# Performance work log

Measured on AMD Instinct MI355X. Metric: run time of the kernel, lower is better.

The kernel has to match this reference:

```python
import jax, jax.numpy as jnp
import numpy as np

NUM_EMBEDDINGS = 1024
EMBEDDING_DIM = 64
COMMITMENT_COST = 0.25
N_TOKENS = 262144


def setup_inputs() -> dict:
    key = jax.random.key(0)
    k1, k2 = jax.random.split(key)
    inputs = jax.random.normal(k1, (N_TOKENS, EMBEDDING_DIM), dtype=jnp.float32)
    # torch init: uniform(-1/K, 1/K)
    lim = 1.0 / NUM_EMBEDDINGS
    codebook = jax.random.uniform(k2, (NUM_EMBEDDINGS, EMBEDDING_DIM),
                                  dtype=jnp.float32, minval=-lim, maxval=lim)
    return {"inputs": inputs, "codebook": codebook}


def reference(inputs, codebook):
    # inputs: [N, D] flat tokens, codebook: [K, D]
    x = inputs.reshape(-1, EMBEDDING_DIM)
    distances = (jnp.sum(x * x, axis=1, keepdims=True)
                 + jnp.sum(codebook * codebook, axis=1)
                 - 2.0 * jnp.matmul(x, codebook.T))
    encoding_indices = jnp.argmin(distances, axis=1)[:, None]  # [N, 1]
    # one-hot @ codebook == gather of nearest code vectors
    quantized = codebook[encoding_indices[:, 0]]  # [N, D]
    e_latent_loss = jnp.mean((jax.lax.stop_gradient(quantized) - x) ** 2)
    q_latent_loss = jnp.mean((quantized - jax.lax.stop_gradient(x)) ** 2)
    loss = q_latent_loss + COMMITMENT_COST * e_latent_loss
    # straight-through estimator
    quantized = x + jax.lax.stop_gradient(quantized - x)
    return quantized, loss, encoding_indices
```

## Files before the change

kernel.cpp:

```cpp
#include <hip/hip_runtime.h>
#include <math.h>

#define NTOK   262144
#define DIM    64
#define NCODE  1024
#define LOSSOFF (NTOK*DIM)
#define IDXOFF  (NTOK*DIM + 1)

#define MARGIN 4e-5f
#define RCAP   65536

#define OFF_BC     0
#define OFF_CBHI   1024
#define OFF_CBMID  33792
#define OFF_RCNT   66560
#define OFF_CORR   66561
#define OFF_RLIST  66562
#define OFF_BLK    132098
#define WS_FLOATS  134146

typedef __attribute__((ext_vector_type(8))) short short8;
typedef __attribute__((ext_vector_type(4))) float f32x4;

#define GLOAD_LDS(g, l) __builtin_amdgcn_global_load_lds(                    \
    (const __attribute__((address_space(1))) void*)(g),                     \
    (__attribute__((address_space(3))) void*)(l), 16, 0, 0)

__device__ __forceinline__ ushort bf16rn(float f) {
    unsigned u = __float_as_uint(f);
    return (ushort)((u + 0x7fffu + ((u >> 16) & 1u)) >> 16);
}
__device__ __forceinline__ float bf16tof(ushort h) {
    return __uint_as_float(((unsigned)h) << 16);
}

__global__ __launch_bounds__(256) void vq_prep_cb(const float* __restrict__ cb,
                                                  float* __restrict__ ws) {
    int c = blockIdx.x * 256 + threadIdx.x;
    if (c == 0) { ((int*)ws)[OFF_RCNT] = 0; ws[OFF_CORR] = 0.f; }
    if (c >= NCODE) return;
    ushort* cbh = (ushort*)(ws + OFF_CBHI);
    ushort* cbm = (ushort*)(ws + OFF_CBMID);
    const float4* p = (const float4*)(cb + (size_t)c * DIM);
    int sw = (c & 7) << 1;
    float a0 = 0.f, a1 = 0.f, a2 = 0.f, a3 = 0.f;
#pragma unroll
    for (int i = 0; i < 16; i++) {
        float4 v = p[i];
        a0 = fmaf(v.x, v.x, a0); a1 = fmaf(v.y, v.y, a1);
        a2 = fmaf(v.z, v.z, a2); a3 = fmaf(v.w, v.w, a3);
        ushort4 h, m;
        h.x = bf16rn(v.x); m.x = bf16rn(v.x - bf16tof(h.x));
        h.y = bf16rn(v.y); m.y = bf16rn(v.y - bf16tof(h.y));
        h.z = bf16rn(v.z); m.z = bf16rn(v.z - bf16tof(h.z));
        h.w = bf16rn(v.w); m.w = bf16rn(v.w - bf16tof(h.w));
        ((ushort4*)(cbh + (size_t)c * 64))[i ^ sw] = h;
        ((ushort4*)(cbm + (size_t)c * 64))[i ^ sw] = m;
    }
    ws[OFF_BC + c] = (a0 + a1) + (a2 + a3);
}

__global__ __launch_bounds__(256)
__attribute__((amdgpu_waves_per_eu(3)))
void vq_mfma(const float* __restrict__ x,
             const float* __restrict__ cbf,
             float* __restrict__ out,
             float* __restrict__ ws) {
    __shared__ uint4 smem[8][256];
    __shared__ int idxs[128];
    __shared__ float red[4];
    const float* Bc = ws + OFF_BC;
    const ushort* cbh = (const ushort*)(ws + OFF_CBHI);
    const ushort* cbm = (const ushort*)(ws + OFF_CBMID);

    int tid = threadIdx.x, lane = tid & 63, wv = tid >> 6;
    int col = lane & 15, q = lane >> 4, q4 = q * 4;
    int tokb = blockIdx.x * 128 + wv * 32;

    short8 Xhi[2][2], Xmid[2][2];
#pragma unroll
    for (int tt = 0; tt < 2; ++tt) {
        int token = tokb + tt * 16 + col;
        const float* xr = x + (size_t)token * 64;
#pragma unroll
        for (int s = 0; s < 2; ++s) {
            float4 v0 = *(const float4*)(xr + s * 32 + q * 8);
            float4 v1 = *(const float4*)(xr + s * 32 + q * 8 + 4);
            float vv[8] = {v0.x, v0.y, v0.z, v0.w, v1.x, v1.y, v1.z, v1.w};
            short8 hv, mv;
#pragma unroll
            for (int j = 0; j < 8; ++j) {
                ushort h = bf16rn(vv[j]);
                float r = vv[j] - bf16tof(h);
                hv[j] = (short)h; mv[j] = (short)bf16rn(r);
            }
            Xhi[tt][s] = hv; Xmid[tt][s] = mv;
        }
    }

    float best[2][4], sec[2][4];
    int bbase[2][4];
#pragma unroll
    for (int tt = 0; tt < 2; ++tt)
#pragma unroll
        for (int rr = 0; rr < 4; ++rr) {
            best[tt][rr] = 3.4e38f; sec[tt][rr] = 3.4e38f; bbase[tt][rr] = 0;
        }

    const ushort* wsrc = (wv < 2 ? cbh : cbm) + (size_t)(wv & 1) * 512 + lane * 8;
    int ro_h0 = col * 8 + ((0 + q) ^ (col & 7));
    int ro_h1 = col * 8 + ((4 + q) ^ (col & 7));
    int ro_m0 = 128 + col * 8 + ((0 + q) ^ (col & 7));
    int ro_m1 = 128 + col * 8 + ((4 + q) ^ (col & 7));

#pragma unroll
    for (int t = 0; t < 4; ++t)
        GLOAD_LDS(wsrc + t * 1024, &smem[t][wv * 64]);
    __syncthreads();

    for (int rd = 0; rd < 16; ++rd) {
        int base = (rd & 1) << 2;
        if (rd < 15) {
            int nb = 4 - base;
            const ushort* ts = wsrc + (size_t)(rd + 1) * 4096;
#pragma unroll
            for (int t = 0; t < 4; ++t)
                GLOAD_LDS(ts + t * 1024, &smem[nb + t][wv * 64]);
        }
#pragma unroll
        for (int sub = 0; sub < 4; ++sub) {
            int c0 = (rd * 4 + sub) * 16;
            float4 bq = *(const float4*)(Bc + c0 + q4);
            short8 Ah0 = *(const short8*)&smem[base + sub][ro_h0];
            short8 Ah1 = *(const short8*)&smem[base + sub][ro_h1];
            short8 Am0 = *(const short8*)&smem[base + sub][ro_m0];
            short8 Am1 = *(const short8*)&smem[base + sub][ro_m1];
            int bv = c0 + q4;
            float bqv[4] = {bq.x, bq.y, bq.z, bq.w};
#pragma unroll
            for (int tt = 0; tt < 2; ++tt) {
                f32x4 acc = {0.f, 0.f, 0.f, 0.f};
                acc = __builtin_amdgcn_mfma_f32_16x16x32_bf16(Ah0, Xhi[tt][0], acc, 0, 0, 0);
                acc = __builtin_amdgcn_mfma_f32_16x16x32_bf16(Ah1, Xhi[tt][1], acc, 0, 0, 0);
                acc = __builtin_amdgcn_mfma_f32_16x16x32_bf16(Ah0, Xmid[tt][0], acc, 0, 0, 0);
                acc = __builtin_amdgcn_mfma_f32_16x16x32_bf16(Ah1, Xmid[tt][1], acc, 0, 0, 0);
                acc = __builtin_amdgcn_mfma_f32_16x16x32_bf16(Am0, Xhi[tt][0], acc, 0, 0, 0);
                acc = __builtin_amdgcn_mfma_f32_16x16x32_bf16(Am1, Xhi[tt][1], acc, 0, 0, 0);
#pragma unroll
                for (int rr = 0; rr < 4; ++rr) {
                    float d = fmaf(-2.f, acc[rr], bqv[rr]);
                    bool lt = d < best[tt][rr];
                    sec[tt][rr] = __builtin_amdgcn_fmed3f(d, best[tt][rr], sec[tt][rr]);
                    best[tt][rr] = fminf(best[tt][rr], d);
                    bbase[tt][rr] = lt ? bv : bbase[tt][rr];
                }
            }
        }
        __syncthreads();
    }

#pragma unroll
    for (int tt = 0; tt < 2; ++tt) {
        float b = best[tt][0], s2 = sec[tt][0];
        int bi = bbase[tt][0];
#pragma unroll
        for (int rr = 1; rr < 4; ++rr) {
            float ob = best[tt][rr];
            int oi = bbase[tt][rr] + rr;
            s2 = fminf(fminf(s2, sec[tt][rr]), fmaxf(b, ob));
            bool lt2 = (ob < b) || (ob == b && oi < bi);
            b = lt2 ? ob : b; bi = lt2 ? oi : bi;
        }
#pragma unroll
        for (int off = 16; off <= 32; off <<= 1) {
            float ob = __shfl_xor(b, off, 64);
            float os = __shfl_xor(s2, off, 64);
            int   oi = __shfl_xor(bi, off, 64);
            s2 = fminf(fminf(s2, os), fmaxf(b, ob));
            bool lt = (ob < b) || (ob == b && oi < bi);
            b = lt ? ob : b; bi = lt ? oi : bi;
        }
        if (lane < 16) {
            int token = tokb + tt * 16 + lane;
            out[IDXOFF + token] = (float)bi;
            idxs[wv * 32 + tt * 16 + lane] = bi;
            if (s2 - b < MARGIN) {
                int pos = atomicAdd((int*)ws + OFF_RCNT, 1);
                if (pos < RCAP) ((int*)ws)[OFF_RLIST + pos] = token;
            }
        }
    }
    __syncthreads();

    float se = 0.f;
    int tokb0 = blockIdx.x * 128;
#pragma unroll
    for (int i = 0; i < 8; ++i) {
        int gi = i * 256 + tid;
        int tok = gi >> 4, qd = gi & 15;
        int ci = idxs[tok];
        float4 xvv = *(const float4*)(x + (size_t)(tokb0 + tok) * 64 + qd * 4);
        float4 qv = *(const float4*)(cbf + (size_t)ci * 64 + qd * 4);
        float d0 = qv.x - xvv.x, d1 = qv.y - xvv.y;
        float d2 = qv.z - xvv.z, d3 = qv.w - xvv.w;
        float4 o;
        o.x = xvv.x + d0; o.y = xvv.y + d1; o.z = xvv.z + d2; o.w = xvv.w + d3;
        *(float4*)(out + (size_t)(tokb0 + tok) * 64 + qd * 4) = o;
        se += d0 * d0 + d1 * d1 + d2 * d2 + d3 * d3;
    }
    for (int off = 32; off; off >>= 1) se += __shfl_down(se, off, 64);
    if (lane == 0) red[wv] = se;
    __syncthreads();
    if (tid == 0) ws[OFF_BLK + blockIdx.x] = (red[0] + red[1]) + (red[2] + red[3]);
}

__global__ __launch_bounds__(256) void vq_refine(const float* __restrict__ x,
                                                 const float* __restrict__ cb,
                                                 float* __restrict__ out,
                                                 float* __restrict__ ws) {
    __shared__ float ctile[128][64];
    __shared__ float xs[8][64];
    __shared__ float As[8];
    __shared__ int   tokid[8], oidx[8], nidx[8];
    __shared__ unsigned long long rkeys[8][128];
    __shared__ float dred[4];

    int cnt = min(((int*)ws)[OFF_RCNT], RCAP);
    if (cnt <= 0) return;
    int ngroups = (cnt + 7) >> 3;
    int tid = threadIdx.x;
    int code = tid & 127, th = tid >> 7;

    for (int grp = blockIdx.x; grp < ngroups; grp += gridDim.x) {
        if (tid < 8) {
            int i = grp * 8 + tid;
            int t = ((int*)ws)[OFF_RLIST + min(i, cnt - 1)];
            tokid[tid] = t;
            oidx[tid] = (int)out[IDXOFF + t];
        }
        __syncthreads();
#pragma unroll
        for (int it = 0; it < 2; ++it) {
            int idx = it * 256 + tid;
            xs[idx >> 6][idx & 63] = x[(size_t)tokid[idx >> 6] * 64 + (idx & 63)];
        }
        __syncthreads();
        if (tid < 8) {
            float a0 = 0.f, a1 = 0.f, a2 = 0.f, a3 = 0.f;
#pragma unroll
            for (int kc = 0; kc < 16; ++kc) {
                float4 xk = *(const float4*)(xs[tid] + kc * 4);
                a0 = fmaf(xk.x, xk.x, a0); a1 = fmaf(xk.y, xk.y, a1);
                a2 = fmaf(xk.z, xk.z, a2); a3 = fmaf(xk.w, xk.w, a3);
            }
            As[tid] = (a0 + a1) + (a2 + a3);
        }

        unsigned long long bk[4] = {~0ull, ~0ull, ~0ull, ~0ull};
        int tb = th * 4;

        for (int pass = 0; pass < 8; ++pass) {
            int cbase = pass * 128;
            __syncthreads();
#pragma unroll
            for (int it = 0; it < 8; ++it) {
                int gi = it * 256 + tid;
                int cc = gi >> 4, qq = gi & 15;
                float4 v = *(const float4*)(cb + (size_t)(cbase + cc) * 64 + qq * 4);
                *(float4*)&ctile[cc][(qq ^ (cc & 15)) * 4] = v;
            }
            __syncthreads();

            float p0 = 0.f, p1 = 0.f, p2 = 0.f, p3 = 0.f;
#pragma unroll
            for (int qq = 0; qq < 16; ++qq) {
                float4 cv = *(const float4*)&ctile[code][(qq ^ (code & 15)) * 4];
                float4 x0 = *(const float4*)(xs[tb + 0] + qq * 4);
                float4 x1 = *(const float4*)(xs[tb + 1] + qq * 4);
                float4 x2 = *(const float4*)(xs[tb + 2] + qq * 4);
                float4 x3 = *(const float4*)(xs[tb + 3] + qq * 4);
                p0 = fmaf(x0.x, cv.x, p0); p0 = fmaf(x0.y, cv.y, p0);
                p0 = fmaf(x0.z, cv.z, p0); p0 = fmaf(x0.w, cv.w, p0);
                p1 = fmaf(x1.x, cv.x, p1); p1 = fmaf(x1.y, cv.y, p1);
                p1 = fmaf(x1.z, cv.z, p1); p1 = fmaf(x1.w, cv.w, p1);
                p2 = fmaf(x2.x, cv.x, p2); p2 = fmaf(x2.y, cv.y, p2);
                p2 = fmaf(x2.z, cv.z, p2); p2 = fmaf(x2.w, cv.w, p2);
                p3 = fmaf(x3.x, cv.x, p3); p3 = fmaf(x3.y, cv.y, p3);
                p3 = fmaf(x3.z, cv.z, p3); p3 = fmaf(x3.w, cv.w, p3);
            }
            float bn = ws[OFF_BC + cbase + code];
            int gcode = cbase + code;
            float pv[4] = {p0, p1, p2, p3};
#pragma unroll
            for (int j = 0; j < 4; ++j) {
                float s = As[tb + j] + bn;
                float d = fmaf(-2.0f, pv[j], s);
                unsigned long long key =
                    (((unsigned long long)__float_as_uint(d)) << 32) | (unsigned)gcode;
                bk[j] = min(bk[j], key);
            }
        }
        __syncthreads();
#pragma unroll
        for (int j = 0; j < 4; ++j) rkeys[tb + j][code] = bk[j];
        __syncthreads();

        int wv2 = tid >> 6, lane = tid & 63;
#pragma unroll
        for (int u = 0; u < 2; ++u) {
            int tt = wv2 * 2 + u;
            unsigned long long k = min(rkeys[tt][lane], rkeys[tt][lane + 64]);
#pragma unroll
            for (int off = 32; off; off >>= 1)
                k = min(k, (unsigned long long)__shfl_xor((long long)k, off, 64));
            if (lane == 0) {
                int ni = (int)(unsigned)(k & 0xffffffffull);
                nidx[tt] = ni;
                if (grp * 8 + tt < cnt) out[IDXOFF + tokid[tt]] = (float)ni;
            }
        }
        __syncthreads();

        float delta = 0.f;
        {
            int tok = tid >> 5, e2 = (tid & 31) * 2;
            if (grp * 8 + tok < cnt) {
                int nw = nidx[tok], od = oidx[tok];
                if (nw != od) {
                    float x0 = xs[tok][e2], x1 = xs[tok][e2 + 1];
                    float qn0 = cb[(size_t)nw * 64 + e2], qn1 = cb[(size_t)nw * 64 + e2 + 1];
                    float qo0 = cb[(size_t)od * 64 + e2], qo1 = cb[(size_t)od * 64 + e2 + 1];
                    float dn0 = qn0 - x0, dn1 = qn1 - x1;
                    float do0 = qo0 - x0, do1 = qo1 - x1;
                    out[(size_t)tokid[tok] * 64 + e2]     = x0 + dn0;
                    out[(size_t)tokid[tok] * 64 + e2 + 1] = x1 + dn1;
                    delta = (dn0 * dn0 + dn1 * dn1) - (do0 * do0 + do1 * do1);
                }
            }
        }
        for (int off = 32; off; off >>= 1) delta += __shfl_down(delta, off, 64);
        if ((tid & 63) == 0) dred[tid >> 6] = delta;
        __syncthreads();
        if (tid == 0) {
            float dsum = (dred[0] + dred[1]) + (dred[2] + dred[3]);
            if (dsum != 0.f) atomicAdd(ws + OFF_CORR, dsum);
        }
        __syncthreads();
    }
}

__global__ __launch_bounds__(256) void vq_loss2(float* __restrict__ out,
                                                const float* __restrict__ ws) {
    const float* blk = ws + OFF_BLK;
    __shared__ double sd[256];
    double s = 0.0;
    for (int i = threadIdx.x; i < 2048; i += 256) s += (double)blk[i];
    sd[threadIdx.x] = s;
    __syncthreads();
    for (int off = 128; off; off >>= 1) {
        if (threadIdx.x < off) sd[threadIdx.x] += sd[threadIdx.x + off];
        __syncthreads();
    }
    if (threadIdx.x == 0) {
        double tot = sd[0] + (double)ws[OFF_CORR];
        out[LOSSOFF] = (float)(1.25 * tot / ((double)NTOK * (double)DIM));
    }
}

extern "C" void kernel_launch(void* const* d_in, const int* in_sizes, int n_in,
                              void* d_out, int out_size, void* d_ws, size_t ws_size,
                              hipStream_t stream) {
    (void)in_sizes; (void)n_in; (void)out_size; (void)ws_size;
    const float* x = (const float*)d_in[0];
    const float* cb = (const float*)d_in[1];
    float* out = (float*)d_out;
    float* ws = (float*)d_ws;

    hipLaunchKernelGGL(vq_prep_cb, dim3(4), dim3(256), 0, stream, cb, ws);
    hipLaunchKernelGGL(vq_mfma, dim3(2048), dim3(256), 0, stream, x, cb, out, ws);
    hipLaunchKernelGGL(vq_refine, dim3(1024), dim3(256), 0, stream, x, cb, out, ws);
    hipLaunchKernelGGL(vq_loss2, dim3(1), dim3(256), 0, stream, out, ws);
}
```

Baseline: 156.0 us.

## Triple-buffer codebook tiles in LDS and stage codebook norms in shared memory

Replaces double buffering of codebook tiles with a three-stage ring, prefetching two rounds ahead and using manual vmcnt waits plus bare barriers in place of full __syncthreads. This lets global-to-LDS loads overlap more MFMA work. The codebook squared norms are also copied once into LDS, so each sub-tile reads them from shared memory instead of global memory. The cost is more LDS per block, which may lower occupancy, and hand-written waitcnt logic that must count outstanding loads correctly.

```diff
diff --git a/kernel.cpp b/kernel.cpp
--- a/kernel.cpp
+++ b/kernel.cpp
@@ -66,7 +66,8 @@
              const float* __restrict__ cbf,
              float* __restrict__ out,
              float* __restrict__ ws) {
-    __shared__ uint4 smem[8][256];
+    __shared__ uint4 smem[12][256];
+    __shared__ float bcs[1024];
     __shared__ int idxs[128];
     __shared__ float red[4];
     const float* Bc = ws + OFF_BC;
@@ -98,6 +99,11 @@
         }
     }
 
+    {
+        float4 b4 = *(const float4*)(Bc + tid * 4);
+        *(float4*)&bcs[tid * 4] = b4;
+    }
+
     float best[2][4], sec[2][4];
     int bbase[2][4];
 #pragma unroll
@@ -116,25 +122,30 @@
 #pragma unroll
     for (int t = 0; t < 4; ++t)
         GLOAD_LDS(wsrc + t * 1024, &smem[t][wv * 64]);
-    __syncthreads();
-
+#pragma unroll
+    for (int t = 0; t < 4; ++t)
+        GLOAD_LDS(wsrc + 4096 + t * 1024, &smem[4 + t][wv * 64]);
+    asm volatile("s_waitcnt vmcnt(4) lgkmcnt(0)" ::: "memory");
+    __builtin_amdgcn_s_barrier();
+
+    int set = 0;
     for (int rd = 0; rd < 16; ++rd) {
-        int base = (rd & 1) << 2;
-        if (rd < 15) {
-            int nb = 4 - base;
-            const ushort* ts = wsrc + (size_t)(rd + 1) * 4096;
+        if (rd + 2 < 16) {
+            int ns = set + 2; if (ns >= 3) ns -= 3;
+            const ushort* ts = wsrc + (size_t)(rd + 2) * 4096;
 #pragma unroll
             for (int t = 0; t < 4; ++t)
-                GLOAD_LDS(ts + t * 1024, &smem[nb + t][wv * 64]);
+                GLOAD_LDS(ts + t * 1024, &smem[ns * 4 + t][wv * 64]);
         }
 #pragma unroll
         for (int sub = 0; sub < 4; ++sub) {
             int c0 = (rd * 4 + sub) * 16;
-            float4 bq = *(const float4*)(Bc + c0 + q4);
-            short8 Ah0 = *(const short8*)&smem[base + sub][ro_h0];
-            short8 Ah1 = *(const short8*)&smem[base + sub][ro_h1];
-            short8 Am0 = *(const short8*)&smem[base + sub][ro_m0];
-            short8 Am1 = *(const short8*)&smem[base + sub][ro_m1];
+            float4 bq = *(const float4*)&bcs[c0 + q4];
+            const uint4* tb = &smem[set * 4 + sub][0];
+            short8 Ah0 = *(const short8*)&tb[ro_h0];
+            short8 Ah1 = *(const short8*)&tb[ro_h1];
+            short8 Am0 = *(const short8*)&tb[ro_m0];
+            short8 Am1 = *(const short8*)&tb[ro_m1];
             int bv = c0 + q4;
             float bqv[4] = {bq.x, bq.y, bq.z, bq.w};
 #pragma unroll
@@ -156,7 +167,10 @@
                 }
             }
         }
-        __syncthreads();
+        if (rd < 14) asm volatile("s_waitcnt vmcnt(4)" ::: "memory");
+        else         asm volatile("s_waitcnt vmcnt(0)" ::: "memory");
+        __builtin_amdgcn_s_barrier();
+        set += 1; if (set >= 3) set -= 3;
     }
 
 #pragma unroll
```

New measurement: 173.6 us. 11.3% more time.

## Drop split-bf16 refinement, use single bf16 MFMA with wider rescoring margin

Applied to the files above, without the earlier changes.

Replaces the three-term bf16 hi/mid split GEMM (six MFMAs per tile) with a single bf16 product (two MFMAs), and widens the near-tie margin so more tokens get exact rescoring. Halves codebook LDS staging, swaps global_load_lds for register-staged loads with a manual swizzle, and raises waves_per_eu occupancy. This cuts matrix-core work and LDS traffic. The lower precision sends more tokens down the fallback rescoring path and risks overflowing its capacity.

```diff
diff --git a/kernel.cpp b/kernel.cpp
--- a/kernel.cpp
+++ b/kernel.cpp
@@ -7,7 +7,7 @@
 #define LOSSOFF (NTOK*DIM)
 #define IDXOFF  (NTOK*DIM + 1)
 
-#define MARGIN 4e-5f
+#define MARGIN 3e-4f
 #define RCAP   65536
 
 #define OFF_BC     0
@@ -22,10 +22,6 @@
 typedef __attribute__((ext_vector_type(8))) short short8;
 typedef __attribute__((ext_vector_type(4))) float f32x4;
 
-#define GLOAD_LDS(g, l) __builtin_amdgcn_global_load_lds(                    \
-    (const __attribute__((address_space(1))) void*)(g),                     \
-    (__attribute__((address_space(3))) void*)(l), 16, 0, 0)
-
 __device__ __forceinline__ ushort bf16rn(float f) {
     unsigned u = __float_as_uint(f);
     return (ushort)((u + 0x7fffu + ((u >> 16) & 1u)) >> 16);
@@ -40,44 +36,38 @@
     if (c == 0) { ((int*)ws)[OFF_RCNT] = 0; ws[OFF_CORR] = 0.f; }
     if (c >= NCODE) return;
     ushort* cbh = (ushort*)(ws + OFF_CBHI);
-    ushort* cbm = (ushort*)(ws + OFF_CBMID);
     const float4* p = (const float4*)(cb + (size_t)c * DIM);
-    int sw = (c & 7) << 1;
     float a0 = 0.f, a1 = 0.f, a2 = 0.f, a3 = 0.f;
 #pragma unroll
     for (int i = 0; i < 16; i++) {
         float4 v = p[i];
         a0 = fmaf(v.x, v.x, a0); a1 = fmaf(v.y, v.y, a1);
         a2 = fmaf(v.z, v.z, a2); a3 = fmaf(v.w, v.w, a3);
-        ushort4 h, m;
-        h.x = bf16rn(v.x); m.x = bf16rn(v.x - bf16tof(h.x));
-        h.y = bf16rn(v.y); m.y = bf16rn(v.y - bf16tof(h.y));
-        h.z = bf16rn(v.z); m.z = bf16rn(v.z - bf16tof(h.z));
-        h.w = bf16rn(v.w); m.w = bf16rn(v.w - bf16tof(h.w));
-        ((ushort4*)(cbh + (size_t)c * 64))[i ^ sw] = h;
-        ((ushort4*)(cbm + (size_t)c * 64))[i ^ sw] = m;
+        ushort4 h;
+        h.x = bf16rn(v.x); h.y = bf16rn(v.y);
+        h.z = bf16rn(v.z); h.w = bf16rn(v.w);
+        ((ushort4*)(cbh + (size_t)c * 64))[i] = h;
     }
     ws[OFF_BC + c] = (a0 + a1) + (a2 + a3);
 }
 
 __global__ __launch_bounds__(256)
-__attribute__((amdgpu_waves_per_eu(3)))
+__attribute__((amdgpu_waves_per_eu(4)))
 void vq_mfma(const float* __restrict__ x,
              const float* __restrict__ cbf,
              float* __restrict__ out,
              float* __restrict__ ws) {
-    __shared__ uint4 smem[8][256];
+    __shared__ uint4 smem[8][128];
     __shared__ int idxs[128];
     __shared__ float red[4];
     const float* Bc = ws + OFF_BC;
     const ushort* cbh = (const ushort*)(ws + OFF_CBHI);
-    const ushort* cbm = (const ushort*)(ws + OFF_CBMID);
 
     int tid = threadIdx.x, lane = tid & 63, wv = tid >> 6;
     int col = lane & 15, q = lane >> 4, q4 = q * 4;
     int tokb = blockIdx.x * 128 + wv * 32;
 
-    short8 Xhi[2][2], Xmid[2][2];
+    short8 Xhi[2][2];
 #pragma unroll
     for (int tt = 0; tt < 2; ++tt) {
         int token = tokb + tt * 16 + col;
@@ -87,14 +77,10 @@
             float4 v0 = *(const float4*)(xr + s * 32 + q * 8);
             float4 v1 = *(const float4*)(xr + s * 32 + q * 8 + 4);
             float vv[8] = {v0.x, v0.y, v0.z, v0.w, v1.x, v1.y, v1.z, v1.w};
-            short8 hv, mv;
-#pragma unroll
-            for (int j = 0; j < 8; ++j) {
-                ushort h = bf16rn(vv[j]);
-                float r = vv[j] - bf16tof(h);
-                hv[j] = (short)h; mv[j] = (short)bf16rn(r);
-            }
-            Xhi[tt][s] = hv; Xmid[tt][s] = mv;
+            short8 hv;
+#pragma unroll
+            for (int j = 0; j < 8; ++j) hv[j] = (short)bf16rn(vv[j]);
+            Xhi[tt][s] = hv;
         }
     }
 
@@ -107,25 +93,32 @@
             best[tt][rr] = 3.4e38f; sec[tt][rr] = 3.4e38f; bbase[tt][rr] = 0;
         }
 
-    const ushort* wsrc = (wv < 2 ? cbh : cbm) + (size_t)(wv & 1) * 512 + lane * 8;
+    int t0 = tid >> 7, e0 = tid & 127, sc = e0 >> 3, g = e0 & 7;
+    int t1 = t0 + 2;
+    const ushort* s0 = cbh + (size_t)(t0 * 16 + sc) * 64 + g * 8;
+    const ushort* s1 = cbh + (size_t)(t1 * 16 + sc) * 64 + g * 8;
+    int wi = sc * 8 + (g ^ (sc & 7));
     int ro_h0 = col * 8 + ((0 + q) ^ (col & 7));
     int ro_h1 = col * 8 + ((4 + q) ^ (col & 7));
-    int ro_m0 = 128 + col * 8 + ((0 + q) ^ (col & 7));
-    int ro_m1 = 128 + col * 8 + ((4 + q) ^ (col & 7));
-
-#pragma unroll
-    for (int t = 0; t < 4; ++t)
-        GLOAD_LDS(wsrc + t * 1024, &smem[t][wv * 64]);
+
+    uint4 r0 = *(const uint4*)(s0);
+    uint4 r1 = *(const uint4*)(s1);
+    smem[t0][wi] = r0; smem[t1][wi] = r1;
+    r0 = *(const uint4*)(s0 + 4096);
+    r1 = *(const uint4*)(s1 + 4096);
     __syncthreads();
 
     for (int rd = 0; rd < 16; ++rd) {
         int base = (rd & 1) << 2;
+        int nb = 4 - base;
         if (rd < 15) {
-            int nb = 4 - base;
-            const ushort* ts = wsrc + (size_t)(rd + 1) * 4096;
-#pragma unroll
-            for (int t = 0; t < 4; ++t)
-                GLOAD_LDS(ts + t * 1024, &smem[nb + t][wv * 64]);
+            smem[nb + t0][wi] = r0;
+            smem[nb + t1][wi] = r1;
+            if (rd < 14) {
+                size_t off = (size_t)(rd + 2) * 4096;
+                r0 = *(const uint4*)(s0 + off);
+                r1 = *(const uint4*)(s1 + off);
+            }
         }
 #pragma unroll
         for (int sub = 0; sub < 4; ++sub) {
@@ -133,8 +126,6 @@
             float4 bq = *(const float4*)(Bc + c0 + q4);
             short8 Ah0 = *(const short8*)&smem[base + sub][ro_h0];
             short8 Ah1 = *(const short8*)&smem[base + sub][ro_h1];
-            short8 Am0 = *(const short8*)&smem[base + sub][ro_m0];
-            short8 Am1 = *(const short8*)&smem[base + sub][ro_m1];
             int bv = c0 + q4;
             float bqv[4] = {bq.x, bq.y, bq.z, bq.w};
 #pragma unroll
@@ -142,10 +133,6 @@
                 f32x4 acc = {0.f, 0.f, 0.f, 0.f};
                 acc = __builtin_amdgcn_mfma_f32_16x16x32_bf16(Ah0, Xhi[tt][0], acc, 0, 0, 0);
                 acc = __builtin_amdgcn_mfma_f32_16x16x32_bf16(Ah1, Xhi[tt][1], acc, 0, 0, 0);
-                acc = __builtin_amdgcn_mfma_f32_16x16x32_bf16(Ah0, Xmid[tt][0], acc, 0, 0, 0);
-                acc = __builtin_amdgcn_mfma_f32_16x16x32_bf16(Ah1, Xmid[tt][1], acc, 0, 0, 0);
-                acc = __builtin_amdgcn_mfma_f32_16x16x32_bf16(Am0, Xhi[tt][0], acc, 0, 0, 0);
-                acc = __builtin_amdgcn_mfma_f32_16x16x32_bf16(Am1, Xhi[tt][1], acc, 0, 0, 0);
 #pragma unroll
                 for (int rr = 0; rr < 4; ++rr) {
                     float d = fmaf(-2.f, acc[rr], bqv[rr]);
```

After: 358.8 us. 2.3x slower.
